# Optimization experiments

Hardware: AMD Instinct MI355X
Metric: run time of the kernel (lower is better)

The kernel has to match this reference:

```python
import jax, jax.numpy as jnp
import numpy as np

T, B, H = 256, 512, 2048

def setup_inputs() -> dict:
    key = jax.random.key(0)
    ks = jax.random.split(key, 10)
    s = 1.0 / np.sqrt(H)  # torch RNN/Linear init scale (values only need to be sane)
    return {
        "initial_input": jax.random.normal(ks[0], (B, 1), jnp.float32),
        "hidden": jax.random.normal(ks[1], (B, H), jnp.float32),
        "targets": jax.random.normal(ks[2], (T, B, 1), jnp.float32),
        "W_ih": jax.random.normal(ks[3], (H, 1), jnp.float32) * s,
        "b_ih": jax.random.normal(ks[4], (H,), jnp.float32) * s,
        "W_hh": jax.random.normal(ks[5], (H, H), jnp.float32) * s,
        "b_hh": jax.random.normal(ks[6], (H,), jnp.float32) * s,
        "W_out": jax.random.normal(ks[7], (1, H), jnp.float32) * s,
        "b_out": jax.random.normal(ks[8], (1,), jnp.float32) * s,
        "tf_mask": jax.random.randint(ks[9], (T,), 0, 2) > 0,  # per-step teacher-force decision
    }

def reference(initial_input, hidden, targets, W_ih, b_ih, W_hh, b_hh, W_out, b_out, tf_mask):
    def step(carry, xs):
        h, x = carry                      # h: [B,H], x: [B,1]
        tgt, tf = xs                      # tgt: [B,1], tf: scalar bool
        h = jnp.tanh(x @ W_ih.T + b_ih + h @ W_hh.T + b_hh)  # [B,H]
        y = h @ W_out.T + b_out           # [B,1]
        x_next = jnp.where(tf, tgt, y)
        return (h, x_next), y
    (_, _), outputs = jax.lax.scan(step, (hidden, initial_input), (targets, tf_mask))
    return outputs  # [T,B,1]
```

## Files before the change

### kernel.cpp

```cpp
#include <hip/hip_runtime.h>

using half8   = __attribute__((ext_vector_type(8))) _Float16;
using f32x16  = __attribute__((ext_vector_type(16))) float;
using float4v = __attribute__((ext_vector_type(4))) float;

#define T_STEPS 256
#define BATCH   512
#define HID     2048
#define KS      128

__device__ __forceinline__ f32x16 zero16() {
  f32x16 z;
#pragma unroll
  for (int r = 0; r < 16; ++r) z[r] = 0.0f;
  return z;
}

__device__ __forceinline__ half8 load16_llc(const half8* p) {
  half8 r;
  asm volatile("global_load_dwordx4 %0, %1, off sc0 sc1" : "=v"(r) : "v"(p));
  return r;
}
__device__ __forceinline__ float loadf_llc(const float* p) {
  float r;
  asm volatile("global_load_dword %0, %1, off sc0 sc1" : "=v"(r) : "v"(p));
  return r;
}
__device__ __forceinline__ void store16_llc(half8* p, half8 v) {
  asm volatile("global_store_dwordx4 %0, %1, off sc0 sc1" :: "v"(p), "v"(v) : "memory");
}
__device__ __forceinline__ void storef_llc(float* p, float v) {
  asm volatile("global_store_dword %0, %1, off sc0 sc1" :: "v"(p), "v"(v) : "memory");
}

__global__ void pack_whh_k(const float* __restrict__ whh, half8* __restrict__ bp) {
  int id   = blockIdx.x * 256 + threadIdx.x;
  int lane = id & 63;
  int ks   = (id >> 6) & 127;
  int nblk = id >> 13;
  int j = nblk * 32 + (lane & 31);
  int k = ks * 16 + (lane >> 5) * 8;
  const float4v* src = (const float4v*)(whh + (size_t)j * HID + k);
  float4v a = src[0], b = src[1];
  half8 v;
  v[0]=(_Float16)a[0]; v[1]=(_Float16)a[1]; v[2]=(_Float16)a[2]; v[3]=(_Float16)a[3];
  v[4]=(_Float16)b[0]; v[5]=(_Float16)b[1]; v[6]=(_Float16)b[2]; v[7]=(_Float16)b[3];
  bp[id] = v;
}

__global__ void pack_h_k(const float* __restrict__ hsrc, half8* __restrict__ hp) {
  int id   = blockIdx.x * 256 + threadIdx.x;
  int lane = id & 63;
  int ks   = (id >> 6) & 127;
  int bblk = id >> 13;
  int b = bblk * 32 + (lane & 31);
  int k = ks * 16 + (lane >> 5) * 8;
  const float4v* src = (const float4v*)(hsrc + (size_t)b * HID + k);
  float4v a = src[0], c = src[1];
  half8 v;
  v[0]=(_Float16)a[0]; v[1]=(_Float16)a[1]; v[2]=(_Float16)a[2]; v[3]=(_Float16)a[3];
  v[4]=(_Float16)c[0]; v[5]=(_Float16)c[1]; v[6]=(_Float16)c[2]; v[7]=(_Float16)c[3];
  hp[id] = v;
}

__global__ void bias_k(const float* __restrict__ bih, const float* __restrict__ bhh,
                       float* __restrict__ bias) {
  int i = blockIdx.x * 256 + threadIdx.x;
  if (i < HID) bias[i] = bih[i] + bhh[i];
}

__global__ void tf_expand_k(const int* __restrict__ tf, int* __restrict__ tfc,
                            unsigned* __restrict__ bar) {
  __shared__ int fmt;
  if (threadIdx.x == 0) {
    const unsigned* u = (const unsigned*)tf;
    int all01 = 1;
    for (int i = 0; i < 32; ++i) if (u[i] > 1u) all01 = 0;
    if (all01) {
      int odd0 = 1;
      for (int i = 1; i < 32; i += 2) if (u[i] != 0u) odd0 = 0;
      fmt = odd0 ? 2 : 1;
    } else fmt = 0;
  }
  __syncthreads();
  int i = threadIdx.x;
  int v;
  if (fmt == 2)      v = tf[2 * i];
  else if (fmt == 1) v = tf[i];
  else               v = (int)((const unsigned char*)tf)[i];
  tfc[i] = v ? 1 : 0;
  bar[i] = 0u;
}

__global__ __launch_bounds__(512) void rnn_persist(
    const float* __restrict__ x0,   const float* __restrict__ tgt,
    const int*   __restrict__ tfc,  const float* __restrict__ wih,
    const float* __restrict__ wout, const float* __restrict__ bias,
    const float* __restrict__ bout, const half8* __restrict__ wp,
    half8* __restrict__ h0,         half8* __restrict__ h1,
    float* __restrict__ ypg,        float* __restrict__ out,
    unsigned* __restrict__ bar) {
  __shared__ float part[4][64][68];
  __shared__ float hs[64][68];
  __shared__ float xs[64];
  __shared__ float ypart[8][64];
  __shared__ float wih_s[64], wout_s[64], bias_s[64];
  __shared__ int   tfs[T_STEPS];

  const int bid = blockIdx.x;
  const int m = bid & 7;
  const int n = bid >> 3;
  const int tid = threadIdx.x;
  const int w = tid >> 6;
  const int l = tid & 63;
  const int hi = l >> 5;
  const int c = l & 31;

  const float bo = bout[0];

  if (tid < 64) {
    int j = n * 64 + tid;
    wih_s[tid]  = wih[j];
    wout_s[tid] = wout[j];
    bias_s[tid] = bias[j];
  }
  if (tid < T_STEPS) tfs[tid] = tfc[tid];

  half8 wb0[16], wb1[16];
  {
    const half8* b0p = wp + ((size_t)(2 * n + 0) * KS + w * 16) * 64 + l;
    const half8* b1p = wp + ((size_t)(2 * n + 1) * KS + w * 16) * 64 + l;
#pragma unroll
    for (int i = 0; i < 16; ++i) { wb0[i] = b0p[i * 64]; wb1[i] = b1p[i * 64]; }
  }
  __syncthreads();

  for (int t = 0; t < T_STEPS; ++t) {
    const half8* hr = (t & 1) ? h1 : h0;
    half8*       hw = (t & 1) ? h0 : h1;

    if (tid < 64) {
      float x;
      if (t == 0) {
        x = x0[m * 64 + tid];
      } else {
        const float* yp = ypg + ((size_t)((t - 1) & 1) * 8 + m) * 2048 + tid;
        float a[32];
#pragma unroll
        for (int i = 0; i < 32; ++i) a[i] = loadf_llc(yp + i * 64);
        asm volatile("s_waitcnt vmcnt(0)" ::: "memory");
        __builtin_amdgcn_sched_barrier(0);
        float s = 0.0f;
#pragma unroll
        for (int i = 0; i < 32; ++i) s += a[i];
        float ysum = s + bo;
        if (n == 0) out[(size_t)(t - 1) * BATCH + m * 64 + tid] = ysum;
        x = tfs[t - 1] ? tgt[(size_t)(t - 1) * BATCH + m * 64 + tid] : ysum;
      }
      xs[tid] = x;
    }

    f32x16 acc00 = zero16(), acc01 = zero16(), acc10 = zero16(), acc11 = zero16();
    {
      const half8* a0p = hr + ((size_t)(2 * m + 0) * KS + w * 16) * 64 + l;
      const half8* a1p = hr + ((size_t)(2 * m + 1) * KS + w * 16) * 64 + l;
#pragma unroll
      for (int kk = 0; kk < 4; ++kk) {
        half8 a0[4], a1[4];
#pragma unroll
        for (int i = 0; i < 4; ++i) {
          a0[i] = load16_llc(a0p + (kk * 4 + i) * 64);
          a1[i] = load16_llc(a1p + (kk * 4 + i) * 64);
        }
        asm volatile("s_waitcnt vmcnt(0)" ::: "memory");
        __builtin_amdgcn_sched_barrier(0);
#pragma unroll
        for (int i = 0; i < 4; ++i) {
          acc00 = __builtin_amdgcn_mfma_f32_32x32x16_f16(a0[i], wb0[kk * 4 + i], acc00, 0, 0, 0);
          acc01 = __builtin_amdgcn_mfma_f32_32x32x16_f16(a0[i], wb1[kk * 4 + i], acc01, 0, 0, 0);
          acc10 = __builtin_amdgcn_mfma_f32_32x32x16_f16(a1[i], wb0[kk * 4 + i], acc10, 0, 0, 0);
          acc11 = __builtin_amdgcn_mfma_f32_32x32x16_f16(a1[i], wb1[kk * 4 + i], acc11, 0, 0, 0);
        }
      }
    }

    if (w < 4) {
#pragma unroll
      for (int r = 0; r < 16; ++r) {
        int row0 = (r & 3) + 8 * (r >> 2) + 4 * hi;
        part[w][row0     ][c     ] = acc00[r];
        part[w][row0     ][c + 32] = acc01[r];
        part[w][row0 + 32][c     ] = acc10[r];
        part[w][row0 + 32][c + 32] = acc11[r];
      }
    }
    __syncthreads();
    if (w >= 4) {
      int ww = w - 4;
#pragma unroll
      for (int r = 0; r < 16; ++r) {
        int row0 = (r & 3) + 8 * (r >> 2) + 4 * hi;
        part[ww][row0     ][c     ] += acc00[r];
        part[ww][row0     ][c + 32] += acc01[r];
        part[ww][row0 + 32][c     ] += acc10[r];
        part[ww][row0 + 32][c + 32] += acc11[r];
      }
    }
    __syncthreads();

    {
      int mb = w & 1, nb = (w >> 1) & 1, rh = w >> 2;
#pragma unroll
      for (int r = 0; r < 8; ++r) {
        int rr = rh * 8 + r;
        int row = mb * 32 + (rr & 3) + 8 * (rr >> 2) + 4 * hi;
        int col = nb * 32 + c;
        float s = part[0][row][col] + part[1][row][col]
                + part[2][row][col] + part[3][row][col];
        s += bias_s[col] + xs[row] * wih_s[col];
        float e = __expf(2.0f * s);
        hs[row][col] = 1.0f - 2.0f / (e + 1.0f);
      }
    }
    __syncthreads();

    {
      int row = tid & 63;
      int g   = tid >> 6;
      float hv[8];
      float4v v0 = *(const float4v*)&hs[row][g * 8];
      float4v v1 = *(const float4v*)&hs[row][g * 8 + 4];
      hv[0]=v0[0]; hv[1]=v0[1]; hv[2]=v0[2]; hv[3]=v0[3];
      hv[4]=v1[0]; hv[5]=v1[1]; hv[6]=v1[2]; hv[7]=v1[3];

      float yp = 0.0f;
#pragma unroll
      for (int e = 0; e < 8; ++e) yp += hv[e] * wout_s[g * 8 + e];
      ypart[g][row] = yp;

      half8 f;
#pragma unroll
      for (int e = 0; e < 8; ++e) f[e] = (_Float16)hv[e];
      int bblk = 2 * m + (row >> 5);
      int ksg  = n * 4 + (g >> 1);
      int lane = (g & 1) * 32 + (row & 31);
      store16_llc(hw + ((size_t)bblk * KS + ksg) * 64 + lane, f);
    }
    __syncthreads();

    if (w == 0) {
      float y = ypart[0][l] + ypart[1][l] + ypart[2][l] + ypart[3][l]
              + ypart[4][l] + ypart[5][l] + ypart[6][l] + ypart[7][l];
      storef_llc(ypg + (((size_t)(t & 1) * 8 + m) * 32 + n) * 64 + l, y);
      asm volatile("s_waitcnt vmcnt(0)" ::: "memory");
    }

    if (tid == 0) {
      __hip_atomic_fetch_add(&bar[m * 32], 1u, __ATOMIC_RELAXED,
                             __HIP_MEMORY_SCOPE_AGENT);
      unsigned tgt_cnt = 32u * (unsigned)(t + 1);
      while (__hip_atomic_load(&bar[m * 32], __ATOMIC_RELAXED,
                               __HIP_MEMORY_SCOPE_AGENT) < tgt_cnt)
        __builtin_amdgcn_s_sleep(1);
    }
    __syncthreads();
  }

  if (n == 0 && tid < 64) {
    const float* yp = ypg + ((size_t)((T_STEPS - 1) & 1) * 8 + m) * 2048 + tid;
    float a[32];
#pragma unroll
    for (int i = 0; i < 32; ++i) a[i] = loadf_llc(yp + i * 64);
    asm volatile("s_waitcnt vmcnt(0)" ::: "memory");
    __builtin_amdgcn_sched_barrier(0);
    float s = 0.0f;
#pragma unroll
    for (int i = 0; i < 32; ++i) s += a[i];
    out[(size_t)(T_STEPS - 1) * BATCH + m * 64 + tid] = s + bo;
  }
}

extern "C" void kernel_launch(void* const* d_in, const int* in_sizes, int n_in,
                              void* d_out, int out_size, void* d_ws, size_t ws_size,
                              hipStream_t stream) {
  (void)in_sizes; (void)n_in; (void)out_size; (void)ws_size;
  const float* x0   = (const float*)d_in[0];
  const float* hid  = (const float*)d_in[1];
  const float* tgt  = (const float*)d_in[2];
  const float* wih  = (const float*)d_in[3];
  const float* bih  = (const float*)d_in[4];
  const float* whh  = (const float*)d_in[5];
  const float* bhh  = (const float*)d_in[6];
  const float* wout = (const float*)d_in[7];
  const float* bout = (const float*)d_in[8];
  const int*   tf   = (const int*)d_in[9];
  float* out = (float*)d_out;

  char* ws = (char*)d_ws;
  half8*    wp   = (half8*)ws;
  half8*    h0   = (half8*)(ws + (8u  << 20));
  half8*    h1   = (half8*)(ws + (10u << 20));
  float*    bias = (float*)(ws + (12u << 20));
  int*      tfc  = (int*)  (ws + (12u << 20) + 8192);
  unsigned* bar  = (unsigned*)(ws + (12u << 20) + 16384);
  float*    ypg  = (float*)(ws + (12u << 20) + 32768);

  pack_whh_k <<<2048, 256, 0, stream>>>(whh, wp);
  pack_h_k   <<<512,  256, 0, stream>>>(hid, h0);
  bias_k     <<<8,    256, 0, stream>>>(bih, bhh, bias);
  tf_expand_k<<<1,    256, 0, stream>>>(tf, tfc, bar);

  rnn_persist<<<256, 512, 0, stream>>>(x0, tgt, tfc, wih, wout, bias, bout,
                                       wp, h0, h1, ypg, out, bar);
}
```

Measured before the change: 2.036 ms.

## Rotate hidden state through eight buffer slots and use cached plain loads

Replaces the two ping-pong hidden-state buffers with a pool of eight generations. Each step now writes a fresh address, so the reads of the recurrent state can be ordinary cacheable global loads instead of sc0/sc1 system-coherent loads with a forced full wait. The intent is to let the compiler schedule the loads alongside the MFMAs and to hit in nearer caches. The risk is stale data: a slot is reused every eight steps, and correctness now depends on per-CU caches not holding an old copy of that slot, which the single acquire fence at kernel entry may not guarantee.

```diff
diff --git a/kernel.cpp b/kernel.cpp
--- a/kernel.cpp
+++ b/kernel.cpp
@@ -8,6 +8,8 @@
 #define BATCH   512
 #define HID     2048
 #define KS      128
+#define HGEN    8
+#define HSLOT   (BATCH * HID / 8)
 
 __device__ __forceinline__ f32x16 zero16() {
   f32x16 z;
@@ -16,11 +18,6 @@
   return z;
 }
 
-__device__ __forceinline__ half8 load16_llc(const half8* p) {
-  half8 r;
-  asm volatile("global_load_dwordx4 %0, %1, off sc0 sc1" : "=v"(r) : "v"(p));
-  return r;
-}
 __device__ __forceinline__ float loadf_llc(const float* p) {
   float r;
   asm volatile("global_load_dword %0, %1, off sc0 sc1" : "=v"(r) : "v"(p));
@@ -97,15 +94,16 @@
     const int*   __restrict__ tfc,  const float* __restrict__ wih,
     const float* __restrict__ wout, const float* __restrict__ bias,
     const float* __restrict__ bout, const half8* __restrict__ wp,
-    half8* __restrict__ h0,         half8* __restrict__ h1,
-    float* __restrict__ ypg,        float* __restrict__ out,
-    unsigned* __restrict__ bar) {
+    half8* __restrict__ hpool,      float* __restrict__ ypg,
+    float* __restrict__ out,        unsigned* __restrict__ bar) {
   __shared__ float part[4][64][68];
   __shared__ float hs[64][68];
   __shared__ float xs[64];
   __shared__ float ypart[8][64];
   __shared__ float wih_s[64], wout_s[64], bias_s[64];
   __shared__ int   tfs[T_STEPS];
+
+  __builtin_amdgcn_fence(__ATOMIC_ACQUIRE, "agent");
 
   const int bid = blockIdx.x;
   const int m = bid & 7;
@@ -136,8 +134,8 @@
   __syncthreads();
 
   for (int t = 0; t < T_STEPS; ++t) {
-    const half8* hr = (t & 1) ? h1 : h0;
-    half8*       hw = (t & 1) ? h0 : h1;
+    const half8* hr = hpool + (size_t)((t + HGEN - 1) % HGEN) * HSLOT;
+    half8*       hw = hpool + (size_t)(t % HGEN) * HSLOT;
 
     if (tid < 64) {
       float x;
@@ -169,11 +167,9 @@
         half8 a0[4], a1[4];
 #pragma unroll
         for (int i = 0; i < 4; ++i) {
-          a0[i] = load16_llc(a0p + (kk * 4 + i) * 64);
-          a1[i] = load16_llc(a1p + (kk * 4 + i) * 64);
+          a0[i] = a0p[(kk * 4 + i) * 64];
+          a1[i] = a1p[(kk * 4 + i) * 64];
         }
-        asm volatile("s_waitcnt vmcnt(0)" ::: "memory");
-        __builtin_amdgcn_sched_barrier(0);
 #pragma unroll
         for (int i = 0; i < 4; ++i) {
           acc00 = __builtin_amdgcn_mfma_f32_32x32x16_f16(a0[i], wb0[kk * 4 + i], acc00, 0, 0, 0);
@@ -297,19 +293,18 @@
   float* out = (float*)d_out;
 
   char* ws = (char*)d_ws;
-  half8*    wp   = (half8*)ws;
-  half8*    h0   = (half8*)(ws + (8u  << 20));
-  half8*    h1   = (half8*)(ws + (10u << 20));
-  float*    bias = (float*)(ws + (12u << 20));
-  int*      tfc  = (int*)  (ws + (12u << 20) + 8192);
-  unsigned* bar  = (unsigned*)(ws + (12u << 20) + 16384);
-  float*    ypg  = (float*)(ws + (12u << 20) + 32768);
+  half8*    wp    = (half8*)ws;
+  half8*    hpool = (half8*)(ws + (8u << 20));
+  float*    bias  = (float*)(ws + (24u << 20));
+  int*      tfc   = (int*)  (ws + (24u << 20) + 8192);
+  unsigned* bar   = (unsigned*)(ws + (24u << 20) + 16384);
+  float*    ypg   = (float*)(ws + (24u << 20) + 32768);
 
   pack_whh_k <<<2048, 256, 0, stream>>>(whh, wp);
-  pack_h_k   <<<512,  256, 0, stream>>>(hid, h0);
+  pack_h_k   <<<512,  256, 0, stream>>>(hid, hpool + (size_t)(HGEN - 1) * HSLOT);
   bias_k     <<<8,    256, 0, stream>>>(bih, bhh, bias);
   tf_expand_k<<<1,    256, 0, stream>>>(tf, tfc, bar);
 
   rnn_persist<<<256, 512, 0, stream>>>(x0, tgt, tfc, wih, wout, bias, bout,
-                                       wp, h0, h1, ypg, out, bar);
-}
+                                       wp, hpool, ypg, out, bar);
+}
```

Measured after the change: 3.128 ms. +53.6%, slower.

## Distribute y-feedback reduction across waves and double-buffer hidden-state loads

Applied to the files above, without the earlier changes.

The serial 32-load y-partial reduction done by wave 0 before the matmul is split so each of the 8 waves loads 4 partials. These loads are issued alongside the hidden-state loads, staged in shared memory, and finished by wave 0 after the first barrier. The hidden-state A-operand loads are also restructured into a double-buffered pipeline with vmcnt(4) waits, so MFMAs overlap the next chunk's loads instead of waiting for each group of 8 loads to fully drain. This shortens the per-step critical path of the persistent loop, at the cost of one extra shared buffer and more registers live at once.

```diff
diff --git a/kernel.cpp b/kernel.cpp
--- a/kernel.cpp
+++ b/kernel.cpp
@@ -104,6 +104,7 @@
   __shared__ float hs[64][68];
   __shared__ float xs[64];
   __shared__ float ypart[8][64];
+  __shared__ float yfb[8][64];
   __shared__ float wih_s[64], wout_s[64], bias_s[64];
   __shared__ int   tfs[T_STEPS];
 
@@ -139,50 +140,49 @@
     const half8* hr = (t & 1) ? h1 : h0;
     half8*       hw = (t & 1) ? h0 : h1;
 
-    if (tid < 64) {
-      float x;
-      if (t == 0) {
-        x = x0[m * 64 + tid];
-      } else {
-        const float* yp = ypg + ((size_t)((t - 1) & 1) * 8 + m) * 2048 + tid;
-        float a[32];
-#pragma unroll
-        for (int i = 0; i < 32; ++i) a[i] = loadf_llc(yp + i * 64);
-        asm volatile("s_waitcnt vmcnt(0)" ::: "memory");
-        __builtin_amdgcn_sched_barrier(0);
-        float s = 0.0f;
-#pragma unroll
-        for (int i = 0; i < 32; ++i) s += a[i];
-        float ysum = s + bo;
-        if (n == 0) out[(size_t)(t - 1) * BATCH + m * 64 + tid] = ysum;
-        x = tfs[t - 1] ? tgt[(size_t)(t - 1) * BATCH + m * 64 + tid] : ysum;
-      }
-      xs[tid] = x;
+    float fb0 = 0.f, fb1 = 0.f, fb2 = 0.f, fb3 = 0.f;
+    if (t > 0) {
+      const float* yp = ypg + ((size_t)((t - 1) & 1) * 8 + m) * 2048 + l;
+      fb0 = loadf_llc(yp + (w * 4 + 0) * 64);
+      fb1 = loadf_llc(yp + (w * 4 + 1) * 64);
+      fb2 = loadf_llc(yp + (w * 4 + 2) * 64);
+      fb3 = loadf_llc(yp + (w * 4 + 3) * 64);
     }
 
     f32x16 acc00 = zero16(), acc01 = zero16(), acc10 = zero16(), acc11 = zero16();
     {
       const half8* a0p = hr + ((size_t)(2 * m + 0) * KS + w * 16) * 64 + l;
       const half8* a1p = hr + ((size_t)(2 * m + 1) * KS + w * 16) * 64 + l;
-#pragma unroll
-      for (int kk = 0; kk < 4; ++kk) {
-        half8 a0[4], a1[4];
-#pragma unroll
-        for (int i = 0; i < 4; ++i) {
-          a0[i] = load16_llc(a0p + (kk * 4 + i) * 64);
-          a1[i] = load16_llc(a1p + (kk * 4 + i) * 64);
+      half8 ha[2][4];
+      ha[0][0] = load16_llc(a0p + 0 * 64);
+      ha[0][1] = load16_llc(a0p + 1 * 64);
+      ha[0][2] = load16_llc(a1p + 0 * 64);
+      ha[0][3] = load16_llc(a1p + 1 * 64);
+#pragma unroll
+      for (int i = 0; i < 8; ++i) {
+        const int cur = i & 1, nxt = cur ^ 1;
+        if (i < 7) {
+          ha[nxt][0] = load16_llc(a0p + (2 * i + 2) * 64);
+          ha[nxt][1] = load16_llc(a0p + (2 * i + 3) * 64);
+          ha[nxt][2] = load16_llc(a1p + (2 * i + 2) * 64);
+          ha[nxt][3] = load16_llc(a1p + (2 * i + 3) * 64);
+          asm volatile("s_waitcnt vmcnt(4)" ::: "memory");
+        } else {
+          asm volatile("s_waitcnt vmcnt(0)" ::: "memory");
         }
-        asm volatile("s_waitcnt vmcnt(0)" ::: "memory");
         __builtin_amdgcn_sched_barrier(0);
-#pragma unroll
-        for (int i = 0; i < 4; ++i) {
-          acc00 = __builtin_amdgcn_mfma_f32_32x32x16_f16(a0[i], wb0[kk * 4 + i], acc00, 0, 0, 0);
-          acc01 = __builtin_amdgcn_mfma_f32_32x32x16_f16(a0[i], wb1[kk * 4 + i], acc01, 0, 0, 0);
-          acc10 = __builtin_amdgcn_mfma_f32_32x32x16_f16(a1[i], wb0[kk * 4 + i], acc10, 0, 0, 0);
-          acc11 = __builtin_amdgcn_mfma_f32_32x32x16_f16(a1[i], wb1[kk * 4 + i], acc11, 0, 0, 0);
-        }
-      }
-    }
+        acc00 = __builtin_amdgcn_mfma_f32_32x32x16_f16(ha[cur][0], wb0[2 * i], acc00, 0, 0, 0);
+        acc01 = __builtin_amdgcn_mfma_f32_32x32x16_f16(ha[cur][0], wb1[2 * i], acc01, 0, 0, 0);
+        acc10 = __builtin_amdgcn_mfma_f32_32x32x16_f16(ha[cur][2], wb0[2 * i], acc10, 0, 0, 0);
+        acc11 = __builtin_amdgcn_mfma_f32_32x32x16_f16(ha[cur][2], wb1[2 * i], acc11, 0, 0, 0);
+        acc00 = __builtin_amdgcn_mfma_f32_32x32x16_f16(ha[cur][1], wb0[2 * i + 1], acc00, 0, 0, 0);
+        acc01 = __builtin_amdgcn_mfma_f32_32x32x16_f16(ha[cur][1], wb1[2 * i + 1], acc01, 0, 0, 0);
+        acc10 = __builtin_amdgcn_mfma_f32_32x32x16_f16(ha[cur][3], wb0[2 * i + 1], acc10, 0, 0, 0);
+        acc11 = __builtin_amdgcn_mfma_f32_32x32x16_f16(ha[cur][3], wb1[2 * i + 1], acc11, 0, 0, 0);
+      }
+    }
+
+    if (t > 0) yfb[w][l] = (fb0 + fb1) + (fb2 + fb3);
 
     if (w < 4) {
 #pragma unroll
@@ -195,6 +195,7 @@
       }
     }
     __syncthreads();
+
     if (w >= 4) {
       int ww = w - 4;
 #pragma unroll
@@ -205,6 +206,18 @@
         part[ww][row0 + 32][c     ] += acc10[r];
         part[ww][row0 + 32][c + 32] += acc11[r];
       }
+    } else if (w == 0) {
+      float x;
+      if (t == 0) {
+        x = x0[m * 64 + l];
+      } else {
+        float s = ((yfb[0][l] + yfb[1][l]) + (yfb[2][l] + yfb[3][l]))
+                + ((yfb[4][l] + yfb[5][l]) + (yfb[6][l] + yfb[7][l]));
+        float ysum = s + bo;
+        if (n == 0) out[(size_t)(t - 1) * BATCH + m * 64 + l] = ysum;
+        x = tfs[t - 1] ? tgt[(size_t)(t - 1) * BATCH + m * 64 + l] : ysum;
+      }
+      xs[l] = x;
     }
     __syncthreads();
 
```

New measurement: 2.046 ms, median of 2. Within noise of the previous version (+0.5%).
